# Performance work log

Hardware: AMD Instinct MI355X
Metric: run time of the kernel (lower is better)

## Reference

```python
import jax, jax.numpy as jnp
import numpy as np

BSZ, SL, K, D = 4, 2048, 24, 512  # batch, seq len, num_eigh, d_out (=d_in)


def _top_hankel_eigh(sl: int, k: int):
    # Hankel matrix Z[i,j] = 2 / ((i+j)^3 - (i+j)), 1-indexed i,j in [sl]
    idx = np.arange(1, sl + 1, dtype=np.float64)
    s = idx[:, None] + idx[None, :]
    Z = 2.0 / (s ** 3 - s)
    evals, evecs = np.linalg.eigh(Z)  # ascending
    eig_vals = jnp.asarray(evals[-k:], dtype=jnp.float32)       # [k]
    eig_vecs = jnp.asarray(evecs[:, -k:], dtype=jnp.float32)    # [sl, k]
    return eig_vals, eig_vecs


def setup_inputs() -> dict:
    key = jax.random.key(0)
    k1, k2 = jax.random.split(key)
    eig_vals, eig_vecs = _top_hankel_eigh(SL, K)
    inputs = jax.random.normal(k1, (BSZ, SL, D), dtype=jnp.float32)
    m_phi = jax.random.normal(k2, (D * K, D), dtype=jnp.float32) * 0.02
    return {"inputs": inputs, "eig_vals": eig_vals, "eig_vecs": eig_vecs, "m_phi": m_phi}


def _compute_x_tilde(inputs, eig_vals, eig_vecs):
    # Causal convolution of each input channel with each Hankel eigenvector,
    # done via FFT: out[b,t,i,d] = sum_{s<=t} v[s,i] * u[b,t-s,d]
    bsz, sl, d = inputs.shape
    k = eig_vals.shape[0]
    n = 2 * sl  # zero-pad to avoid circular wraparound
    V_f = jnp.fft.rfft(eig_vecs, n=n, axis=0)          # [n//2+1, k]
    U_f = jnp.fft.rfft(inputs, n=n, axis=1)            # [bsz, n//2+1, d]
    prod = V_f[None, :, :, None] * U_f[:, :, None, :]  # [bsz, n//2+1, k, d]
    conv = jnp.fft.irfft(prod, n=n, axis=1)[:, :sl]    # [bsz, sl, k, d]
    x_tilde = conv * (eig_vals ** 0.25)[None, None, :, None]
    return x_tilde.reshape(bsz, sl, k * d)             # [bsz, sl, k*d]


def reference(inputs, eig_vals, eig_vecs, m_phi):
    # dropout layers are identity in eval / p=0
    x_tilde = _compute_x_tilde(inputs, eig_vals, eig_vecs)
    return x_tilde @ m_phi                             # [bsz, sl, d_out]
```

## Files before the change

kernel.cpp:

```cpp
#include <hip/hip_runtime.h>

typedef _Float16 f16;
typedef _Float16 f16x8 __attribute__((ext_vector_type(8)));
typedef float    f32x4 __attribute__((ext_vector_type(4)));

#define BSZ 4
#define SL  2048
#define NK  24
#define DD  512
#define NPP 134
#define KI  8

typedef const void GV __attribute__((address_space(1)));
typedef void       LV __attribute__((address_space(3)));

__device__ __forceinline__ void gload_lds16(const void* gp, void* lp) {
  __builtin_amdgcn_global_load_lds((GV*)gp, (LV*)lp, 16, 0, 0);
}

__global__ void k_afrag(const float* __restrict__ eig_vals,
                        const float* __restrict__ eig_vecs,
                        f16* __restrict__ afrag) {
  int i = blockIdx.x, pp = blockIdx.y;
  int l = threadIdx.x;
  float sc = sqrtf(sqrtf(eig_vals[i]));
  int base = 2047 - 16 * (pp - 6) - (l & 15) + 8 * (l >> 4);
  f16 tmp[8];
#pragma unroll
  for (int j = 0; j < 8; ++j) {
    int x = base + j;
    float v = (x >= 0 && x < SL) ? eig_vecs[(size_t)(SL - 1 - x) * NK + i] * sc : 0.f;
    tmp[j] = (f16)v;
  }
  *(f16x8*)(afrag + (((size_t)i * NPP + pp) * 64 + l) * 8) = *(const f16x8*)tmp;
}

__global__ void k_tu(const float* __restrict__ u, f16* __restrict__ ut) {
  __shared__ float tile[32][33];
  int b = blockIdx.z;
  int s0 = blockIdx.x * 32, d0 = blockIdx.y * 32;
  int tx = threadIdx.x, ty = threadIdx.y;
#pragma unroll
  for (int r = 0; r < 4; ++r) {
    int s = s0 + ty * 4 + r;
    tile[ty * 4 + r][tx] = u[((size_t)b * SL + s) * DD + d0 + tx];
  }
  __syncthreads();
#pragma unroll
  for (int r = 0; r < 4; ++r) {
    int d = d0 + ty * 4 + r;
    ut[((size_t)b * DD + d) * SL + s0 + tx] = (f16)tile[tx][ty * 4 + r];
  }
}

__global__ void k_tm(const float* __restrict__ mp, f16* __restrict__ mht) {
  __shared__ float tile[32][33];
  int k0 = blockIdx.x * 32, e0 = blockIdx.y * 32;
  int tx = threadIdx.x, ty = threadIdx.y;
#pragma unroll
  for (int r = 0; r < 4; ++r)
    tile[ty * 4 + r][tx] = mp[(size_t)(k0 + ty * 4 + r) * DD + e0 + tx];
  __syncthreads();
#pragma unroll
  for (int r = 0; r < 4; ++r)
    mht[(size_t)(e0 + ty * 4 + r) * (NK * DD) + k0 + tx] = (f16)tile[tx][ty * 4 + r];
}

__global__ __launch_bounds__(256, 2) void k_conv(
    const f16* __restrict__ ut, const f16* __restrict__ afrag,
    f16* __restrict__ xt, int ibase) {
  __shared__ f16 bt[3][256 * 32];
  const int tid = threadIdx.x;
  const int lin = blockIdx.x + (blockIdx.y << 5) + (blockIdx.z << 8);
  const int tb = (lin >> 6) & 15;
  const int dh = lin & 1;
  const int iL = (lin >> 1) & 7;
  const int b  = (lin >> 4) & 3;
  const int iG = ibase + iL;
  const int t0 = tb * 128;

  const int w = tid >> 6, l = tid & 63;
  const int l15 = l & 15, lq = l >> 4;
  const int stage_col = ((l & 3) ^ ((l >> 3) & 3)) * 8;
  const int stage_row = l >> 2;
  const int rd_x = (lq ^ ((l15 >> 1) & 3)) * 16;

  const f16* utb = ut + (size_t)b * DD * SL;
  const f16* afi = afrag + ((size_t)iG * NPP * 64 + l) * 8;

  auto stage = [&](int buf, int s0) {
#pragma unroll
    for (int j = 0; j < 4; ++j) {
      int row = w * 64 + j * 16 + stage_row;
      gload_lds16(utb + (size_t)(dh * 256 + row) * SL + s0 + stage_col,
                  &bt[buf][(w * 64 + j * 16) * 32]);
    }
  };

  f32x4 acc[8][4];
#pragma unroll
  for (int m = 0; m < 8; ++m)
#pragma unroll
    for (int n = 0; n < 4; ++n) acc[m][n] = (f32x4){0.f, 0.f, 0.f, 0.f};

  const int nIter = 4 * (tb + 1);
  int pp0 = 8 * tb + 6;

  stage(0, 0);
  stage(1, 32);
  asm volatile("s_waitcnt vmcnt(4)" ::: "memory");
  __builtin_amdgcn_s_barrier();
  __builtin_amdgcn_sched_barrier(0);

  for (int it = 0; it < nIter; ++it) {
    const int bufR = it % 3;
    f16x8 B[4];
#pragma unroll
    for (int n = 0; n < 4; ++n) {
      int row = w * 64 + n * 16 + l15;
      B[n] = *(const f16x8*)((const char*)&bt[bufR][0] + row * 64 + rd_x);
    }
    f16x8 A[8];
#pragma unroll
    for (int m = 0; m < 8; ++m)
      A[m] = *(const f16x8*)(afi + (size_t)(pp0 + m) * 512);

    if (it + 2 < nIter) stage((it + 2) % 3, (it + 2) * 32);

    asm volatile("s_waitcnt vmcnt(12)" ::: "memory");
    __builtin_amdgcn_s_barrier();
    __builtin_amdgcn_sched_barrier(0);

    __builtin_amdgcn_s_setprio(1);
#pragma unroll
    for (int m = 0; m < 8; ++m)
#pragma unroll
      for (int n = 0; n < 4; ++n)
        acc[m][n] = __builtin_amdgcn_mfma_f32_16x16x32_f16(A[m], B[n], acc[m][n], 0, 0, 0);
    __builtin_amdgcn_s_setprio(0);
    pp0 -= 2;
  }

  const size_t rowlen = (size_t)KI * DD;
  const int dbase = dh * 256 + w * 64;
#pragma unroll
  for (int m = 0; m < 8; ++m) {
    int t = t0 + m * 16 + lq * 4;
#pragma unroll
    for (int n = 0; n < 4; ++n) {
      int d = dbase + n * 16 + l15;
      f16* dst = xt + ((size_t)(b * SL + t) * KI + iL) * DD + d;
#pragma unroll
      for (int r = 0; r < 4; ++r)
        dst[(size_t)r * rowlen] = (f16)acc[m][n][r];
    }
  }
}

__global__ __launch_bounds__(256, 2) void k_gemm(
    const f16* __restrict__ xt, const f16* __restrict__ mht,
    float* __restrict__ out, int kc0, int beta) {
  __shared__ f16 at[3][64 * 64];
  __shared__ f16 btl[3][128 * 64];
  const int AK = KI * DD;
  const int tid = threadIdx.x;
  const int n0 = blockIdx.x * 128;
  const int m0 = blockIdx.y * 64;
  const int w = tid >> 6, l = tid & 63;
  const int l15 = l & 15, lq = l >> 4;
  const int wm = w >> 1, wn = w & 1;
  const int stage_col = ((l & 7) ^ (l >> 3)) * 8;
  const int stage_row = l >> 3;

  auto stage = [&](int buf, int k0) {
#pragma unroll
    for (int j = 0; j < 2; ++j) {
      int row = (w * 2 + j) * 8 + stage_row;
      gload_lds16(xt + (size_t)(m0 + row) * AK + k0 + stage_col,
                  &at[buf][(w * 2 + j) * 8 * 64]);
    }
#pragma unroll
    for (int j = 0; j < 4; ++j) {
      int row = (w * 4 + j) * 8 + stage_row;
      gload_lds16(mht + (size_t)(n0 + row) * (NK * DD) + kc0 + k0 + stage_col,
                  &btl[buf][(w * 4 + j) * 8 * 64]);
    }
  };

  f32x4 acc[2][4];
#pragma unroll
  for (int m = 0; m < 2; ++m)
#pragma unroll
    for (int n = 0; n < 4; ++n) acc[m][n] = (f32x4){0.f, 0.f, 0.f, 0.f};

  const int nIter = AK / 64;
  stage(0, 0);
  stage(1, 64);
  asm volatile("s_waitcnt vmcnt(6)" ::: "memory");
  __builtin_amdgcn_s_barrier();
  __builtin_amdgcn_sched_barrier(0);

  for (int it = 0; it < nIter; ++it) {
    const int bufR = it % 3;
    f16x8 Af[2][2], Bf[2][4];
#pragma unroll
    for (int ks = 0; ks < 2; ++ks) {
#pragma unroll
      for (int m = 0; m < 2; ++m) {
        int lin2 = (wm * 32 + m * 16 + l15) * 128 + ks * 64 + lq * 16;
        lin2 ^= (l15 & 7) << 4;
        Af[ks][m] = *(const f16x8*)((const char*)&at[bufR][0] + lin2);
      }
#pragma unroll
      for (int n = 0; n < 4; ++n) {
        int lin2 = (wn * 64 + n * 16 + l15) * 128 + ks * 64 + lq * 16;
        lin2 ^= (l15 & 7) << 4;
        Bf[ks][n] = *(const f16x8*)((const char*)&btl[bufR][0] + lin2);
      }
    }

    if (it + 2 < nIter) stage((it + 2) % 3, (it + 2) * 64);

    asm volatile("s_waitcnt vmcnt(6)" ::: "memory");
    __builtin_amdgcn_s_barrier();
    __builtin_amdgcn_sched_barrier(0);

    __builtin_amdgcn_s_setprio(1);
#pragma unroll
    for (int ks = 0; ks < 2; ++ks)
#pragma unroll
      for (int m = 0; m < 2; ++m)
#pragma unroll
        for (int n = 0; n < 4; ++n)
          acc[m][n] = __builtin_amdgcn_mfma_f32_16x16x32_f16(
              Af[ks][m], Bf[ks][n], acc[m][n], 0, 0, 0);
    __builtin_amdgcn_s_setprio(0);
  }

#pragma unroll
  for (int m = 0; m < 2; ++m) {
    int row = m0 + wm * 32 + m * 16 + lq * 4;
#pragma unroll
    for (int n = 0; n < 4; ++n) {
      int e = n0 + wn * 64 + n * 16 + l15;
      float* dst = out + (size_t)row * DD + e;
#pragma unroll
      for (int r = 0; r < 4; ++r) {
        float v = acc[m][n][r];
        if (beta) v += dst[(size_t)r * DD];
        dst[(size_t)r * DD] = v;
      }
    }
  }
}

extern "C" void kernel_launch(void* const* d_in, const int* in_sizes, int n_in,
                              void* d_out, int out_size, void* d_ws, size_t ws_size,
                              hipStream_t stream) {
  const float* u    = (const float*)d_in[0];
  const float* ev   = (const float*)d_in[1];
  const float* evec = (const float*)d_in[2];
  const float* mp   = (const float*)d_in[3];
  float* out = (float*)d_out;
  char* ws = (char*)d_ws;

  const size_t UT_OFF  = 0;
  const size_t MHT_OFF = 8388608;
  const size_t AF_OFF  = 20971520;
  const size_t XT_OFF  = 24264704;

  f16* ut    = (f16*)(ws + UT_OFF);
  f16* mht   = (f16*)(ws + MHT_OFF);
  f16* afrag = (f16*)(ws + AF_OFF);
  f16* xt    = (f16*)(ws + XT_OFF);

  k_afrag<<<dim3(24, NPP), 64, 0, stream>>>(ev, evec, afrag);
  k_tu<<<dim3(SL / 32, DD / 32, BSZ), dim3(32, 8), 0, stream>>>(u, ut);
  k_tm<<<dim3((NK * DD) / 32, DD / 32), dim3(32, 8), 0, stream>>>(mp, mht);

  for (int c = 0; c < NK / KI; ++c) {
    k_conv<<<dim3(32, KI, BSZ), 256, 0, stream>>>(ut, afrag, xt, c * KI);
    k_gemm<<<dim3(DD / 128, (BSZ * SL) / 64), 256, 0, stream>>>(
        xt, mht, out, c * KI * DD, c > 0);
  }
}
```

Before: 428.5 us.

## Reuse Toeplitz A fragments across half-steps and double-buffer 64-wide conv stages

The conv kernel now processes two 32-wide s-chunks per iteration, using double-buffered LDS (2x2 halves) instead of a 3-deep ring. Because the Toeplitz A fragments shift by two panels per half-step, it loads only 4 new fragments per iteration and rotates the register window, instead of reloading 8 fragments for each 32-chunk. This removes half the global A loads and halves the number of barriers. In exchange, launch bounds drop to one block per SIMD group with more registers, and the larger LDS footprint lowers occupancy.

```diff
diff --git a/kernel.cpp b/kernel.cpp
--- a/kernel.cpp
+++ b/kernel.cpp
@@ -66,10 +66,10 @@
     mht[(size_t)(e0 + ty * 4 + r) * (NK * DD) + k0 + tx] = (f16)tile[tx][ty * 4 + r];
 }
 
-__global__ __launch_bounds__(256, 2) void k_conv(
+__global__ __launch_bounds__(256, 1) void k_conv(
     const f16* __restrict__ ut, const f16* __restrict__ afrag,
     f16* __restrict__ xt, int ibase) {
-  __shared__ f16 bt[3][256 * 32];
+  __shared__ f16 bt[2][2][256 * 32];
   const int tid = threadIdx.x;
   const int lin = blockIdx.x + (blockIdx.y << 5) + (blockIdx.z << 8);
   const int tb = (lin >> 6) & 15;
@@ -88,12 +88,12 @@
   const f16* utb = ut + (size_t)b * DD * SL;
   const f16* afi = afrag + ((size_t)iG * NPP * 64 + l) * 8;
 
-  auto stage = [&](int buf, int s0) {
+  auto stage_half = [&](int p, int h, int s0) {
 #pragma unroll
     for (int j = 0; j < 4; ++j) {
       int row = w * 64 + j * 16 + stage_row;
       gload_lds16(utb + (size_t)(dh * 256 + row) * SL + s0 + stage_col,
-                  &bt[buf][(w * 64 + j * 16) * 32]);
+                  &bt[p][h][(w * 64 + j * 16) * 32]);
     }
   };
 
@@ -103,42 +103,72 @@
 #pragma unroll
     for (int n = 0; n < 4; ++n) acc[m][n] = (f32x4){0.f, 0.f, 0.f, 0.f};
 
-  const int nIter = 4 * (tb + 1);
+  const int nIter = 2 * (tb + 1);
   int pp0 = 8 * tb + 6;
 
-  stage(0, 0);
-  stage(1, 32);
-  asm volatile("s_waitcnt vmcnt(4)" ::: "memory");
+  stage_half(0, 0, 0);
+  stage_half(0, 1, 32);
+  f16x8 A[8];
+#pragma unroll
+  for (int m = 0; m < 8; ++m)
+    A[m] = *(const f16x8*)(afi + (size_t)(pp0 + m) * 512);
+  asm volatile("s_waitcnt vmcnt(0)" ::: "memory");
   __builtin_amdgcn_s_barrier();
   __builtin_amdgcn_sched_barrier(0);
 
   for (int it = 0; it < nIter; ++it) {
-    const int bufR = it % 3;
-    f16x8 B[4];
+    const int p = it & 1;
+    if (it + 1 < nIter) {
+      stage_half(p ^ 1, 0, (it + 1) * 64);
+      stage_half(p ^ 1, 1, (it + 1) * 64 + 32);
+    }
+    int q1 = pp0 - 1; if (q1 < 0) q1 = 0;
+    int q2 = pp0 - 2; if (q2 < 0) q2 = 0;
+    int q3 = pp0 - 3; if (q3 < 0) q3 = 0;
+    int q4 = pp0 - 4; if (q4 < 0) q4 = 0;
+    f16x8 fp1 = *(const f16x8*)(afi + (size_t)q1 * 512);
+    f16x8 fp2 = *(const f16x8*)(afi + (size_t)q2 * 512);
+    f16x8 fp3 = *(const f16x8*)(afi + (size_t)q3 * 512);
+    f16x8 fp4 = *(const f16x8*)(afi + (size_t)q4 * 512);
+
+    f16x8 B0[4];
 #pragma unroll
     for (int n = 0; n < 4; ++n) {
       int row = w * 64 + n * 16 + l15;
-      B[n] = *(const f16x8*)((const char*)&bt[bufR][0] + row * 64 + rd_x);
-    }
-    f16x8 A[8];
+      B0[n] = *(const f16x8*)((const char*)&bt[p][0][0] + row * 64 + rd_x);
+    }
+    __builtin_amdgcn_s_setprio(1);
 #pragma unroll
     for (int m = 0; m < 8; ++m)
-      A[m] = *(const f16x8*)(afi + (size_t)(pp0 + m) * 512);
-
-    if (it + 2 < nIter) stage((it + 2) % 3, (it + 2) * 32);
-
-    asm volatile("s_waitcnt vmcnt(12)" ::: "memory");
+#pragma unroll
+      for (int n = 0; n < 4; ++n)
+        acc[m][n] = __builtin_amdgcn_mfma_f32_16x16x32_f16(A[m], B0[n], acc[m][n], 0, 0, 0);
+    __builtin_amdgcn_s_setprio(0);
+
+    f16x8 B1[4];
+#pragma unroll
+    for (int n = 0; n < 4; ++n) {
+      int row = w * 64 + n * 16 + l15;
+      B1[n] = *(const f16x8*)((const char*)&bt[p][1][0] + row * 64 + rd_x);
+    }
+    __builtin_amdgcn_s_setprio(1);
+#pragma unroll
+    for (int n = 0; n < 4; ++n) {
+      acc[0][n] = __builtin_amdgcn_mfma_f32_16x16x32_f16(fp2,  B1[n], acc[0][n], 0, 0, 0);
+      acc[1][n] = __builtin_amdgcn_mfma_f32_16x16x32_f16(fp1,  B1[n], acc[1][n], 0, 0, 0);
+#pragma unroll
+      for (int m = 2; m < 8; ++m)
+        acc[m][n] = __builtin_amdgcn_mfma_f32_16x16x32_f16(A[m - 2], B1[n], acc[m][n], 0, 0, 0);
+    }
+    __builtin_amdgcn_s_setprio(0);
+
+    asm volatile("s_waitcnt vmcnt(4)" ::: "memory");
     __builtin_amdgcn_s_barrier();
     __builtin_amdgcn_sched_barrier(0);
 
-    __builtin_amdgcn_s_setprio(1);
-#pragma unroll
-    for (int m = 0; m < 8; ++m)
-#pragma unroll
-      for (int n = 0; n < 4; ++n)
-        acc[m][n] = __builtin_amdgcn_mfma_f32_16x16x32_f16(A[m], B[n], acc[m][n], 0, 0, 0);
-    __builtin_amdgcn_s_setprio(0);
-    pp0 -= 2;
+    A[7] = A[3]; A[6] = A[2]; A[5] = A[1]; A[4] = A[0];
+    A[3] = fp1;  A[2] = fp2;  A[1] = fp3;  A[0] = fp4;
+    pp0 -= 4;
   }
 
   const size_t rowlen = (size_t)KI * DD;
```

After: 530.6 us. 1.24x slower.

## Reuse shifted Toeplitz A-fragments in conv and load GEMM B directly from global

Applied to the files above, without the earlier changes.

In the convolution kernel, the loop is unrolled by two and A fragments are carried in registers across iterations as a sliding window. Only two new fragments are loaded per half-step instead of eight, which cuts global loads of the Toeplitz eigenvector fragments. In the GEMM kernel, the B operand (transposed m_phi) is no longer staged through LDS. Each wave loads B fragments straight from global into registers, double-buffered, and occupancy is lowered to one block per SM. This trades LDS traffic and barriers for more register pressure and uncoalesced-ish global reads, and odd-iteration/boundary handling via clamped indices risks correctness edge cases.

```diff
diff --git a/kernel.cpp b/kernel.cpp
--- a/kernel.cpp
+++ b/kernel.cpp
@@ -107,27 +107,31 @@
   int pp0 = 8 * tb + 6;
 
   stage(0, 0);
+  f16x8 A[8];
+#pragma unroll
+  for (int m = 0; m < 8; ++m)
+    A[m] = *(const f16x8*)(afi + (size_t)(pp0 + m) * 512);
   stage(1, 32);
   asm volatile("s_waitcnt vmcnt(4)" ::: "memory");
   __builtin_amdgcn_s_barrier();
   __builtin_amdgcn_sched_barrier(0);
 
-  for (int it = 0; it < nIter; ++it) {
-    const int bufR = it % 3;
-    f16x8 B[4];
+  int ra = 0;
+  for (int it = 0; it < nIter; it += 2) {
+    f16x8 B0[4];
 #pragma unroll
     for (int n = 0; n < 4; ++n) {
       int row = w * 64 + n * 16 + l15;
-      B[n] = *(const f16x8*)((const char*)&bt[bufR][0] + row * 64 + rd_x);
-    }
-    f16x8 A[8];
-#pragma unroll
-    for (int m = 0; m < 8; ++m)
-      A[m] = *(const f16x8*)(afi + (size_t)(pp0 + m) * 512);
-
-    if (it + 2 < nIter) stage((it + 2) % 3, (it + 2) * 32);
-
-    asm volatile("s_waitcnt vmcnt(12)" ::: "memory");
+      B0[n] = *(const f16x8*)((const char*)&bt[ra][0] + row * 64 + rd_x);
+    }
+    int ppn = pp0 - 2; if (ppn < 0) ppn = 0;
+    const f16* fpt = afi + (size_t)ppn * 512;
+    f16x8 f0 = *(const f16x8*)fpt;
+    f16x8 f1 = *(const f16x8*)(fpt + 512);
+    int sa = ra + 2; if (sa >= 3) sa -= 3;
+    if (it + 2 < nIter) stage(sa, (it + 2) * 32);
+
+    asm volatile("s_waitcnt vmcnt(6)" ::: "memory");
     __builtin_amdgcn_s_barrier();
     __builtin_amdgcn_sched_barrier(0);
 
@@ -136,9 +140,41 @@
     for (int m = 0; m < 8; ++m)
 #pragma unroll
       for (int n = 0; n < 4; ++n)
-        acc[m][n] = __builtin_amdgcn_mfma_f32_16x16x32_f16(A[m], B[n], acc[m][n], 0, 0, 0);
+        acc[m][n] = __builtin_amdgcn_mfma_f32_16x16x32_f16(A[m], B0[n], acc[m][n], 0, 0, 0);
     __builtin_amdgcn_s_setprio(0);
-    pp0 -= 2;
+
+    int rb = ra + 1; if (rb >= 3) rb -= 3;
+    f16x8 B1[4];
+#pragma unroll
+    for (int n = 0; n < 4; ++n) {
+      int row = w * 64 + n * 16 + l15;
+      B1[n] = *(const f16x8*)((const char*)&bt[rb][0] + row * 64 + rd_x);
+    }
+    int pp2 = pp0 - 4; if (pp2 < 0) pp2 = 0;
+    const f16* gpt = afi + (size_t)pp2 * 512;
+    f16x8 g0 = *(const f16x8*)gpt;
+    f16x8 g1 = *(const f16x8*)(gpt + 512);
+    if (it + 3 < nIter) stage(ra, (it + 3) * 32);
+
+    asm volatile("s_waitcnt vmcnt(6)" ::: "memory");
+    __builtin_amdgcn_s_barrier();
+    __builtin_amdgcn_sched_barrier(0);
+
+    __builtin_amdgcn_s_setprio(1);
+#pragma unroll
+    for (int n = 0; n < 4; ++n) {
+      acc[0][n] = __builtin_amdgcn_mfma_f32_16x16x32_f16(f0, B1[n], acc[0][n], 0, 0, 0);
+      acc[1][n] = __builtin_amdgcn_mfma_f32_16x16x32_f16(f1, B1[n], acc[1][n], 0, 0, 0);
+#pragma unroll
+      for (int m = 2; m < 8; ++m)
+        acc[m][n] = __builtin_amdgcn_mfma_f32_16x16x32_f16(A[m - 2], B1[n], acc[m][n], 0, 0, 0);
+    }
+    __builtin_amdgcn_s_setprio(0);
+
+    A[7] = A[3]; A[6] = A[2]; A[5] = A[1]; A[4] = A[0];
+    A[3] = f1;   A[2] = f0;   A[1] = g1;   A[0] = g0;
+    pp0 -= 4;
+    ra = rb + 1; if (ra >= 3) ra -= 3;
   }
 
   const size_t rowlen = (size_t)KI * DD;
@@ -157,17 +193,17 @@
   }
 }
 
-__global__ __launch_bounds__(256, 2) void k_gemm(
+__global__ __launch_bounds__(256, 1) void k_gemm(
     const f16* __restrict__ xt, const f16* __restrict__ mht,
     float* __restrict__ out, int kc0, int beta) {
   __shared__ f16 at[3][64 * 64];
-  __shared__ f16 btl[3][128 * 64];
   const int AK = KI * DD;
   const int tid = threadIdx.x;
   const int n0 = blockIdx.x * 128;
   const int m0 = blockIdx.y * 64;
   const int w = tid >> 6, l = tid & 63;
   const int l15 = l & 15, lq = l >> 4;
+  const int k8 = lq << 3;
   const int wm = w >> 1, wn = w & 1;
   const int stage_col = ((l & 7) ^ (l >> 3)) * 8;
   const int stage_row = l >> 3;
@@ -179,49 +215,56 @@
       gload_lds16(xt + (size_t)(m0 + row) * AK + k0 + stage_col,
                   &at[buf][(w * 2 + j) * 8 * 64]);
     }
-#pragma unroll
-    for (int j = 0; j < 4; ++j) {
-      int row = (w * 4 + j) * 8 + stage_row;
-      gload_lds16(mht + (size_t)(n0 + row) * (NK * DD) + kc0 + k0 + stage_col,
-                  &btl[buf][(w * 4 + j) * 8 * 64]);
-    }
   };
 
-  f32x4 acc[2][4];
-#pragma unroll
-  for (int m = 0; m < 2; ++m)
-#pragma unroll
-    for (int n = 0; n < 4; ++n) acc[m][n] = (f32x4){0.f, 0.f, 0.f, 0.f};
-
-  const int nIter = AK / 64;
-  stage(0, 0);
-  stage(1, 64);
-  asm volatile("s_waitcnt vmcnt(6)" ::: "memory");
-  __builtin_amdgcn_s_barrier();
-  __builtin_amdgcn_sched_barrier(0);
-
-  for (int it = 0; it < nIter; ++it) {
-    const int bufR = it % 3;
-    f16x8 Af[2][2], Bf[2][4];
-#pragma unroll
-    for (int ks = 0; ks < 2; ++ks) {
+  const f16* pB[4];
+#pragma unroll
+  for (int n = 0; n < 4; ++n)
+    pB[n] = mht + (size_t)(n0 + wn * 64 + n * 16 + l15) * (NK * DD) + kc0 + k8;
+
+  auto rdA = [&](int buf, f16x8 (&Af)[2][2]) {
+#pragma unroll
+    for (int ks = 0; ks < 2; ++ks)
 #pragma unroll
       for (int m = 0; m < 2; ++m) {
         int lin2 = (wm * 32 + m * 16 + l15) * 128 + ks * 64 + lq * 16;
         lin2 ^= (l15 & 7) << 4;
-        Af[ks][m] = *(const f16x8*)((const char*)&at[bufR][0] + lin2);
+        Af[ks][m] = *(const f16x8*)((const char*)&at[buf][0] + lin2);
       }
-#pragma unroll
-      for (int n = 0; n < 4; ++n) {
-        int lin2 = (wn * 64 + n * 16 + l15) * 128 + ks * 64 + lq * 16;
-        lin2 ^= (l15 & 7) << 4;
-        Bf[ks][n] = *(const f16x8*)((const char*)&btl[bufR][0] + lin2);
-      }
-    }
-
+  };
+
+  f32x4 acc[2][4];
+#pragma unroll
+  for (int m = 0; m < 2; ++m)
+#pragma unroll
+    for (int n = 0; n < 4; ++n) acc[m][n] = (f32x4){0.f, 0.f, 0.f, 0.f};
+
+  f16x8 BgA[2][4], BgB[2][4];
+
+  stage(0, 0);
+  stage(1, 64);
+#pragma unroll
+  for (int ks = 0; ks < 2; ++ks)
+#pragma unroll
+    for (int n = 0; n < 4; ++n)
+      BgA[ks][n] = *(const f16x8*)(pB[n] + ks * 32);
+  asm volatile("s_waitcnt vmcnt(0)" ::: "memory");
+  __builtin_amdgcn_s_barrier();
+  __builtin_amdgcn_sched_barrier(0);
+
+  const int nIter = AK / 64;
+  for (int it = 0; it < nIter; it += 2) {
+    const int r0 = it % 3;
+    f16x8 Af[2][2];
+    rdA(r0, Af);
+#pragma unroll
+    for (int ks = 0; ks < 2; ++ks)
+#pragma unroll
+      for (int n = 0; n < 4; ++n)
+        BgB[ks][n] = *(const f16x8*)(pB[n] + (it + 1) * 64 + ks * 32);
     if (it + 2 < nIter) stage((it + 2) % 3, (it + 2) * 64);
 
-    asm volatile("s_waitcnt vmcnt(6)" ::: "memory");
+    asm volatile("s_waitcnt vmcnt(10)" ::: "memory");
     __builtin_amdgcn_s_barrier();
     __builtin_amdgcn_sched_barrier(0);
 
@@ -233,7 +276,32 @@
 #pragma unroll
         for (int n = 0; n < 4; ++n)
           acc[m][n] = __builtin_amdgcn_mfma_f32_16x16x32_f16(
-              Af[ks][m], Bf[ks][n], acc[m][n], 0, 0, 0);
+              Af[ks][m], BgA[ks][n], acc[m][n], 0, 0, 0);
+    __builtin_amdgcn_s_setprio(0);
+
+    const int r1 = (it + 1) % 3;
+    f16x8 Af2[2][2];
+    rdA(r1, Af2);
+#pragma unroll
+    for (int ks = 0; ks < 2; ++ks)
+#pragma unroll
+      for (int n = 0; n < 4; ++n)
+        BgA[ks][n] = *(const f16x8*)(pB[n] + (it + 2) * 64 + ks * 32);
+    if (it + 3 < nIter) stage((it + 3) % 3, (it + 3) * 64);
+
+    asm volatile("s_waitcnt vmcnt(10)" ::: "memory");
+    __builtin_amdgcn_s_barrier();
+    __builtin_amdgcn_sched_barrier(0);
+
+    __builtin_amdgcn_s_setprio(1);
+#pragma unroll
+    for (int ks = 0; ks < 2; ++ks)
+#pragma unroll
+      for (int m = 0; m < 2; ++m)
+#pragma unroll
+        for (int n = 0; n < 4; ++n)
+          acc[m][n] = __builtin_amdgcn_mfma_f32_16x16x32_f16(
+              Af2[ks][m], BgB[ks][n], acc[m][n], 0, 0, 0);
     __builtin_amdgcn_s_setprio(0);
   }
 
```

After: 621.7 us. +45.1%, slower.

## Reuse Toeplitz A fragments across iterations via register sliding window in conv

Applied to the files above, without the earlier changes.

The conv kernel previously reloaded all 8 A fragments from global memory every iteration, even though the Toeplitz structure shifts them by only two positions per step. The loop is now unrolled by two and keeps a sliding window of A fragments in registers. Only two new fragments are loaded per half-step, and the rest are rotated in place. This cuts global/L2 traffic and outstanding loads, so the vmcnt waits are tightened. The cost is extra register moves and the assumption that nIter is even, which holds because it is a multiple of 4.

```diff
diff --git a/kernel.cpp b/kernel.cpp
--- a/kernel.cpp
+++ b/kernel.cpp
@@ -107,27 +107,31 @@
   int pp0 = 8 * tb + 6;
 
   stage(0, 0);
+  f16x8 A[8];
+#pragma unroll
+  for (int m = 0; m < 8; ++m)
+    A[m] = *(const f16x8*)(afi + (size_t)(pp0 + m) * 512);
   stage(1, 32);
   asm volatile("s_waitcnt vmcnt(4)" ::: "memory");
   __builtin_amdgcn_s_barrier();
   __builtin_amdgcn_sched_barrier(0);
 
-  for (int it = 0; it < nIter; ++it) {
-    const int bufR = it % 3;
-    f16x8 B[4];
+  int ra = 0;
+  for (int it = 0; it < nIter; it += 2) {
+    f16x8 B0[4];
 #pragma unroll
     for (int n = 0; n < 4; ++n) {
       int row = w * 64 + n * 16 + l15;
-      B[n] = *(const f16x8*)((const char*)&bt[bufR][0] + row * 64 + rd_x);
-    }
-    f16x8 A[8];
-#pragma unroll
-    for (int m = 0; m < 8; ++m)
-      A[m] = *(const f16x8*)(afi + (size_t)(pp0 + m) * 512);
-
-    if (it + 2 < nIter) stage((it + 2) % 3, (it + 2) * 32);
-
-    asm volatile("s_waitcnt vmcnt(12)" ::: "memory");
+      B0[n] = *(const f16x8*)((const char*)&bt[ra][0] + row * 64 + rd_x);
+    }
+    int ppn = pp0 - 2; if (ppn < 0) ppn = 0;
+    const f16* fpt = afi + (size_t)ppn * 512;
+    f16x8 f0 = *(const f16x8*)fpt;
+    f16x8 f1 = *(const f16x8*)(fpt + 512);
+    int sa = ra + 2; if (sa >= 3) sa -= 3;
+    if (it + 2 < nIter) stage(sa, (it + 2) * 32);
+
+    asm volatile("s_waitcnt vmcnt(6)" ::: "memory");
     __builtin_amdgcn_s_barrier();
     __builtin_amdgcn_sched_barrier(0);
 
@@ -136,9 +140,41 @@
     for (int m = 0; m < 8; ++m)
 #pragma unroll
       for (int n = 0; n < 4; ++n)
-        acc[m][n] = __builtin_amdgcn_mfma_f32_16x16x32_f16(A[m], B[n], acc[m][n], 0, 0, 0);
+        acc[m][n] = __builtin_amdgcn_mfma_f32_16x16x32_f16(A[m], B0[n], acc[m][n], 0, 0, 0);
     __builtin_amdgcn_s_setprio(0);
-    pp0 -= 2;
+
+    int rb = ra + 1; if (rb >= 3) rb -= 3;
+    f16x8 B1[4];
+#pragma unroll
+    for (int n = 0; n < 4; ++n) {
+      int row = w * 64 + n * 16 + l15;
+      B1[n] = *(const f16x8*)((const char*)&bt[rb][0] + row * 64 + rd_x);
+    }
+    int pp2 = pp0 - 4; if (pp2 < 0) pp2 = 0;
+    const f16* gpt = afi + (size_t)pp2 * 512;
+    f16x8 g0 = *(const f16x8*)gpt;
+    f16x8 g1 = *(const f16x8*)(gpt + 512);
+    if (it + 3 < nIter) stage(ra, (it + 3) * 32);
+
+    asm volatile("s_waitcnt vmcnt(6)" ::: "memory");
+    __builtin_amdgcn_s_barrier();
+    __builtin_amdgcn_sched_barrier(0);
+
+    __builtin_amdgcn_s_setprio(1);
+#pragma unroll
+    for (int n = 0; n < 4; ++n) {
+      acc[0][n] = __builtin_amdgcn_mfma_f32_16x16x32_f16(f0, B1[n], acc[0][n], 0, 0, 0);
+      acc[1][n] = __builtin_amdgcn_mfma_f32_16x16x32_f16(f1, B1[n], acc[1][n], 0, 0, 0);
+#pragma unroll
+      for (int m = 2; m < 8; ++m)
+        acc[m][n] = __builtin_amdgcn_mfma_f32_16x16x32_f16(A[m - 2], B1[n], acc[m][n], 0, 0, 0);
+    }
+    __builtin_amdgcn_s_setprio(0);
+
+    A[7] = A[3]; A[6] = A[2]; A[5] = A[1]; A[4] = A[0];
+    A[3] = f1;   A[2] = f0;   A[1] = g1;   A[0] = g0;
+    pp0 -= 4;
+    ra = rb + 1; if (ra >= 3) ra -= 3;
   }
 
   const size_t rowlen = (size_t)KI * DD;
```

Result: faster. 397.4 us (-7.3%).
